# Kernel optimization log

Hardware: AMD Instinct MI355X
Metric: run time of the kernel (lower is better)

Reference implementation:

```python
import jax, jax.numpy as jnp
import numpy as np

def setup_inputs() -> dict:
    key = jax.random.key(0)
    k0, k1, k2, k3 = jax.random.split(key, 4)
    B, L, D, E, Dg = 2, 2048, 2048, 8, 256  # Dg = D // E
    x = jax.random.normal(k0, (B, L, D), dtype=jnp.float32)
    Wg = jax.random.normal(k1, (E, D), dtype=jnp.float32) * 0.02     # gate: Linear(D, E)
    Wd = jax.random.normal(k2, (E, Dg, D), dtype=jnp.float32) * 0.02  # down: Linear(D, Dg) per expert
    Wu = jax.random.normal(k3, (E, D, Dg), dtype=jnp.float32) * 0.02  # up:   Linear(Dg, D) per expert
    return {"x": x, "Wg": Wg, "Wd": Wd, "Wu": Wu, "k": 2}

def reference(x, Wg, Wd, Wu, k):
    B, L, D = x.shape
    E = Wg.shape[0]
    T = B * L
    xf = x.reshape(T, D)
    # gate scores: sigmoid(x @ Wg^T), then top-k gate values G and expert indices I
    S = jax.nn.sigmoid(xf @ Wg.T)            # [T, E]
    G, I = jax.lax.top_k(S, k)               # [T, k], [T, k]
    # combine weights per token per expert (zero for unselected experts);
    # equivalent to the original's one_hot + per-expert gather/scatter-add.
    w = jnp.zeros((T, E), x.dtype).at[jnp.arange(T)[:, None], I].add(G)  # [T, E]
    # down: sum_e w[t,e] * (Wd[e] @ x[t])
    down = jnp.einsum('te,egd,td->tg', w, Wd, xf)   # [T, Dg]
    # inner model is identity
    # up: sum_e w[t,e] * (Wu[e] @ down[t])
    up = jnp.einsum('te,edg,tg->td', w, Wu, down)   # [T, D]
    return up.reshape(B, L, D)
```

## Files before the change

### kernel.cpp

```cpp
#include <hip/hip_runtime.h>
#include <hip/hip_bf16.h>
#include <stdint.h>

#define T_TOK 4096
#define DIM   2048
#define NEXP  8
#define DG    256
#define TOPK  2

#define BM 64
#define BN 128
#define BK 32
#define NROWS  (T_TOK*TOPK + NEXP*BM)
#define NBLK_M (NROWS/BM)

typedef __attribute__((ext_vector_type(8))) short short8;
typedef __attribute__((ext_vector_type(4))) float f32x4;

static __device__ __forceinline__ short f2bf(float f) {
    union { float f; uint32_t u; } v{f};
    uint32_t r = v.u + 0x7fffu + ((v.u >> 16) & 1u);
    return (short)(r >> 16);
}
static __device__ __forceinline__ float b2f(short s) {
    union { uint32_t u; float f; } v{((uint32_t)(unsigned short)s) << 16};
    return v.f;
}

#define GLD16(g, l) \
    __builtin_amdgcn_global_load_lds((const __attribute__((address_space(1))) void*)(g), \
                                     (__attribute__((address_space(3))) void*)(l), 16, 0, 0)

__global__ __launch_bounds__(256) void gate_kernel(const float* __restrict__ x,
                                                   const float* __restrict__ Wg,
                                                   int* __restrict__ gidx,
                                                   float* __restrict__ gval,
                                                   short* __restrict__ x_bf)
{
    int token = blockIdx.x * 4 + (threadIdx.x >> 6);
    int lane  = threadIdx.x & 63;
    const float4* xr = (const float4*)(x + (size_t)token * DIM);

    float4 xv[8];
#pragma unroll
    for (int i = 0; i < 8; i++) xv[i] = xr[lane + 64 * i];

    short4* xb = (short4*)(x_bf + (size_t)token * DIM);
#pragma unroll
    for (int i = 0; i < 8; i++) {
        short4 o;
        o.x = f2bf(xv[i].x); o.y = f2bf(xv[i].y);
        o.z = f2bf(xv[i].z); o.w = f2bf(xv[i].w);
        xb[lane + 64 * i] = o;
    }

    float acc[NEXP];
#pragma unroll
    for (int e = 0; e < NEXP; e++) {
        const float4* wr = (const float4*)(Wg + e * DIM);
        float a = 0.0f;
#pragma unroll
        for (int i = 0; i < 8; i++) {
            float4 w = wr[lane + 64 * i];
            a += xv[i].x * w.x + xv[i].y * w.y + xv[i].z * w.z + xv[i].w * w.w;
        }
        acc[e] = a;
    }

#pragma unroll
    for (int m = 1; m < 64; m <<= 1) {
#pragma unroll
        for (int e = 0; e < NEXP; e++) acc[e] += __shfl_xor(acc[e], m, 64);
    }

    if (lane == 0) {
        float sg[NEXP];
#pragma unroll
        for (int e = 0; e < NEXP; e++) sg[e] = 1.0f / (1.0f + expf(-acc[e]));
        int i0 = 0;
#pragma unroll
        for (int e = 1; e < NEXP; e++) if (sg[e] > sg[i0]) i0 = e;
        int i1 = (i0 == 0) ? 1 : 0;
#pragma unroll
        for (int e = 0; e < NEXP; e++) if (e != i0 && e != i1 && sg[e] > sg[i1]) i1 = e;
        gidx[2 * token + 0] = i0;
        gidx[2 * token + 1] = i1;
        gval[2 * token + 0] = sg[i0];
        gval[2 * token + 1] = sg[i1];
    }
}

__global__ __launch_bounds__(256) void convW_kernel(const float* __restrict__ Wd,
                                                    const float* __restrict__ Wu,
                                                    short* __restrict__ Wd_bf,
                                                    short* __restrict__ Wu_bf,
                                                    int n4)
{
    int i = blockIdx.x * 256 + threadIdx.x;
    const float* s; short* d; int j;
    if (i < n4)      { s = Wd; d = Wd_bf; j = i; }
    else             { s = Wu; d = Wu_bf; j = i - n4; if (j >= n4) return; }
    float4 v = ((const float4*)s)[j];
    short4 o;
    o.x = f2bf(v.x); o.y = f2bf(v.y); o.z = f2bf(v.z); o.w = f2bf(v.w);
    ((short4*)d)[j] = o;
}

__global__ __launch_bounds__(1024) void bucket_kernel(const int* __restrict__ gidx,
                                                      int* __restrict__ rowtok,
                                                      int* __restrict__ rowpos,
                                                      int* __restrict__ seg_off)
{
    __shared__ int cnt[NEXP];
    __shared__ int cur[NEXP];
    int tid = threadIdx.x;
    if (tid < NEXP) cnt[tid] = 0;
    __syncthreads();

    for (int t = tid; t < T_TOK; t += 1024) {
        atomicAdd(&cnt[gidx[2 * t + 0]], 1);
        atomicAdd(&cnt[gidx[2 * t + 1]], 1);
    }
    __syncthreads();

    if (tid == 0) {
        int o = 0;
        for (int e = 0; e < NEXP; e++) {
            seg_off[e] = o;
            cur[e] = o;
            o += ((cnt[e] + BM - 1) / BM) * BM;
        }
        seg_off[NEXP] = o;
    }
    __syncthreads();

    for (int r = tid; r < NROWS; r += 1024) rowtok[r] = -1;
    __syncthreads();

    for (int t = tid; t < T_TOK; t += 1024) {
        for (int s = 0; s < TOPK; s++) {
            int e = gidx[2 * t + s];
            int p = atomicAdd(&cur[e], 1);
            rowtok[p] = t;
            rowpos[2 * t + s] = p;
        }
    }
}

template<int K, int Ntot>
__global__ __launch_bounds__(256) void gemm_kernel(const short* __restrict__ A,
                                                   const short* __restrict__ B,
                                                   const int* __restrict__ rowtok,
                                                   const int* __restrict__ seg_off,
                                                   short* __restrict__ C)
{
    __shared__ short As[BM][BK];
    __shared__ short Bs[BN][BK];

    int row0 = blockIdx.x * BM;
    int total = seg_off[NEXP];
    if (row0 >= total) return;
    int e = 0;
    while (row0 >= seg_off[e + 1]) ++e;
    int n0 = blockIdx.y * BN;

    int tid = threadIdx.x;
    int w = tid >> 6, l = tid & 63;

    int ar = (w << 4) + (l >> 2);
    int achunk = (l & 3) ^ ((l >> 3) & 3);
    int ta = rowtok[row0 + ar]; if (ta < 0) ta = 0;
    const short* ag  = A + (size_t)ta * K + achunk * 8;

    const short* be  = B + (size_t)e * Ntot * K + (size_t)n0 * K;
    const short* bg0 = be + (size_t)(((w * 2 + 0) << 4) + (l >> 2)) * K + achunk * 8;
    const short* bg1 = be + (size_t)(((w * 2 + 1) << 4) + (l >> 2)) * K + achunk * 8;

    auto ldsA  = (__attribute__((address_space(3))) void*)&As[w << 4][0];
    auto ldsB0 = (__attribute__((address_space(3))) void*)&Bs[(w * 2 + 0) << 4][0];
    auto ldsB1 = (__attribute__((address_space(3))) void*)&Bs[(w * 2 + 1) << 4][0];

    int mlane = l & 15, qlane = l >> 4;
    int rchunk = ((qlane ^ ((l >> 1) & 3)) << 3);
    int wm = w >> 1, wn = w & 1;
    const short* pA0 = &As[wm * 32 + mlane][rchunk];
    const short* pA1 = pA0 + 16 * BK;
    const short* pB0 = &Bs[wn * 64 + mlane][rchunk];
    const short* pB1 = pB0 + 16 * BK;
    const short* pB2 = pB0 + 32 * BK;
    const short* pB3 = pB0 + 48 * BK;

    f32x4 acc[2][4] = {};

    for (int k0 = 0; k0 < K; k0 += BK) {
        GLD16(ag, ldsA);
        GLD16(bg0, ldsB0);
        GLD16(bg1, ldsB1);
        ag += BK; bg0 += BK; bg1 += BK;
        __syncthreads();

        short8 a0 = *(const short8*)pA0;
        short8 a1 = *(const short8*)pA1;
        short8 b0 = *(const short8*)pB0;
        short8 b1 = *(const short8*)pB1;
        short8 b2 = *(const short8*)pB2;
        short8 b3 = *(const short8*)pB3;

        acc[0][0] = __builtin_amdgcn_mfma_f32_16x16x32_bf16(a0, b0, acc[0][0], 0, 0, 0);
        acc[0][1] = __builtin_amdgcn_mfma_f32_16x16x32_bf16(a0, b1, acc[0][1], 0, 0, 0);
        acc[0][2] = __builtin_amdgcn_mfma_f32_16x16x32_bf16(a0, b2, acc[0][2], 0, 0, 0);
        acc[0][3] = __builtin_amdgcn_mfma_f32_16x16x32_bf16(a0, b3, acc[0][3], 0, 0, 0);
        acc[1][0] = __builtin_amdgcn_mfma_f32_16x16x32_bf16(a1, b0, acc[1][0], 0, 0, 0);
        acc[1][1] = __builtin_amdgcn_mfma_f32_16x16x32_bf16(a1, b1, acc[1][1], 0, 0, 0);
        acc[1][2] = __builtin_amdgcn_mfma_f32_16x16x32_bf16(a1, b2, acc[1][2], 0, 0, 0);
        acc[1][3] = __builtin_amdgcn_mfma_f32_16x16x32_bf16(a1, b3, acc[1][3], 0, 0, 0);
        __syncthreads();
    }

#pragma unroll
    for (int i = 0; i < 2; i++) {
        int rbase = row0 + wm * 32 + i * 16 + qlane * 4;
#pragma unroll
        for (int j = 0; j < 4; j++) {
            int col = n0 + wn * 64 + j * 16 + mlane;
#pragma unroll
            for (int r = 0; r < 4; r++)
                C[(size_t)(rbase + r) * Ntot + col] = f2bf(acc[i][j][r]);
        }
    }
}

__global__ __launch_bounds__(256) void combine1_kernel(const short* __restrict__ dr,
                                                       const int* __restrict__ rowpos,
                                                       const float* __restrict__ gval,
                                                       short* __restrict__ dt)
{
    int t = blockIdx.x, d = threadIdx.x;
    int   p0 = rowpos[2 * t], p1 = rowpos[2 * t + 1];
    float g0 = gval[2 * t],   g1 = gval[2 * t + 1];
    float v = g0 * b2f(dr[(size_t)p0 * DG + d]) + g1 * b2f(dr[(size_t)p1 * DG + d]);
    dt[(size_t)t * DG + d] = f2bf(v);
}

__global__ __launch_bounds__(256) void combine2_kernel(const short* __restrict__ ur,
                                                       const int* __restrict__ rowpos,
                                                       const float* __restrict__ gval,
                                                       float* __restrict__ out)
{
    int i = blockIdx.x * 256 + threadIdx.x;
    int t = i >> 9;
    int c = (i & 511) * 4;
    int   p0 = rowpos[2 * t], p1 = rowpos[2 * t + 1];
    float g0 = gval[2 * t],   g1 = gval[2 * t + 1];
    short4 u0 = *(const short4*)&ur[(size_t)p0 * DIM + c];
    short4 u1 = *(const short4*)&ur[(size_t)p1 * DIM + c];
    float4 o;
    o.x = g0 * b2f(u0.x) + g1 * b2f(u1.x);
    o.y = g0 * b2f(u0.y) + g1 * b2f(u1.y);
    o.z = g0 * b2f(u0.z) + g1 * b2f(u1.z);
    o.w = g0 * b2f(u0.w) + g1 * b2f(u1.w);
    *(float4*)&out[(size_t)t * DIM + c] = o;
}

extern "C" void kernel_launch(void* const* d_in, const int* in_sizes, int n_in,
                              void* d_out, int out_size, void* d_ws, size_t ws_size,
                              hipStream_t stream) {
    const float* x  = (const float*)d_in[0];
    const float* Wg = (const float*)d_in[1];
    const float* Wd = (const float*)d_in[2];
    const float* Wu = (const float*)d_in[3];
    float* out = (float*)d_out;

    char* p = (char*)d_ws;
    int*   gidx    = (int*)(p + 0);
    float* gval    = (float*)(p + 32768);
    int*   rowtok  = (int*)(p + 65536);
    int*   rowpos  = (int*)(p + 100352);
    int*   seg_off = (int*)(p + 133120);
    short* x_bf    = (short*)(p + 133376);
    short* Wd_bf   = (short*)(p + 133376 + 16777216);
    short* Wu_bf   = Wd_bf + 4194304;
    short* dr_bf   = Wu_bf + 4194304;
    short* dt_bf   = dr_bf + (size_t)NROWS * DG;
    short* ur_bf   = dt_bf + (size_t)T_TOK * DG;

    const int W4 = NEXP * DG * DIM / 4;
    gate_kernel<<<T_TOK / 4, 256, 0, stream>>>(x, Wg, gidx, gval, x_bf);
    convW_kernel<<<(2 * W4 + 255) / 256, 256, 0, stream>>>(Wd, Wu, Wd_bf, Wu_bf, W4);
    bucket_kernel<<<1, 1024, 0, stream>>>(gidx, rowtok, rowpos, seg_off);

    gemm_kernel<DIM, DG><<<dim3(NBLK_M, DG / BN), 256, 0, stream>>>(x_bf, Wd_bf, rowtok, seg_off, dr_bf);
    combine1_kernel<<<T_TOK, 256, 0, stream>>>(dr_bf, rowpos, gval, dt_bf);
    gemm_kernel<DG, DIM><<<dim3(NBLK_M, DIM / BN), 256, 0, stream>>>(dt_bf, Wu_bf, rowtok, seg_off, ur_bf);
    combine2_kernel<<<T_TOK * DIM / 4 / 256, 256, 0, stream>>>(ur_bf, rowpos, gval, out);
}
```

Before: 198.9 us.

## Convert weights to bf16 inside GEMM, enlarge M tile, split-K the down GEMM

Removes the separate fp32-to-bf16 weight conversion kernel. Both GEMMs now load fp32 weights through registers and pack them to bf16 while storing to LDS, with a one-step register prefetch. The M tile doubles to 128 rows, so each block computes 4x4 MFMA tiles. The down GEMM is split along K into four fp32 partial planes that the combine1 kernel sums. This saves a full weight-conversion pass and exposes more parallelism in the K=2048 GEMM. The cost is extra fp32 partial traffic, register-path weight loads instead of direct-to-LDS loads, and more padding rows per expert.

```diff
diff --git a/kernel.cpp b/kernel.cpp
--- a/kernel.cpp
+++ b/kernel.cpp
@@ -8,11 +8,12 @@
 #define DG    256
 #define TOPK  2
 
-#define BM 64
+#define BM 128
 #define BN 128
 #define BK 32
 #define NROWS  (T_TOK*TOPK + NEXP*BM)
 #define NBLK_M (NROWS/BM)
+#define KSPLIT 4
 
 typedef __attribute__((ext_vector_type(8))) short short8;
 typedef __attribute__((ext_vector_type(4))) float f32x4;
@@ -25,6 +26,12 @@
 static __device__ __forceinline__ float b2f(short s) {
     union { uint32_t u; float f; } v{((uint32_t)(unsigned short)s) << 16};
     return v.f;
+}
+static __device__ __forceinline__ short8 pack8(float4 a, float4 b) {
+    short8 o;
+    o[0] = f2bf(a.x); o[1] = f2bf(a.y); o[2] = f2bf(a.z); o[3] = f2bf(a.w);
+    o[4] = f2bf(b.x); o[5] = f2bf(b.y); o[6] = f2bf(b.z); o[7] = f2bf(b.w);
+    return o;
 }
 
 #define GLD16(g, l) \
@@ -88,22 +95,6 @@
         gval[2 * token + 0] = sg[i0];
         gval[2 * token + 1] = sg[i1];
     }
-}
-
-__global__ __launch_bounds__(256) void convW_kernel(const float* __restrict__ Wd,
-                                                    const float* __restrict__ Wu,
-                                                    short* __restrict__ Wd_bf,
-                                                    short* __restrict__ Wu_bf,
-                                                    int n4)
-{
-    int i = blockIdx.x * 256 + threadIdx.x;
-    const float* s; short* d; int j;
-    if (i < n4)      { s = Wd; d = Wd_bf; j = i; }
-    else             { s = Wu; d = Wu_bf; j = i - n4; if (j >= n4) return; }
-    float4 v = ((const float4*)s)[j];
-    short4 o;
-    o.x = f2bf(v.x); o.y = f2bf(v.y); o.z = f2bf(v.z); o.w = f2bf(v.w);
-    ((short4*)d)[j] = o;
 }
 
 __global__ __launch_bounds__(1024) void bucket_kernel(const int* __restrict__ gidx,
@@ -147,99 +138,124 @@
     }
 }
 
-template<int K, int Ntot>
+template<int K, int KC, int Ntot, bool PART>
 __global__ __launch_bounds__(256) void gemm_kernel(const short* __restrict__ A,
-                                                   const short* __restrict__ B,
+                                                   const float* __restrict__ Bf,
                                                    const int* __restrict__ rowtok,
                                                    const int* __restrict__ seg_off,
-                                                   short* __restrict__ C)
+                                                   short* __restrict__ Cbf,
+                                                   float* __restrict__ Cf32)
 {
     __shared__ short As[BM][BK];
     __shared__ short Bs[BN][BK];
 
     int row0 = blockIdx.x * BM;
-    int total = seg_off[NEXP];
-    if (row0 >= total) return;
+    if (row0 >= seg_off[NEXP]) return;
     int e = 0;
     while (row0 >= seg_off[e + 1]) ++e;
     int n0 = blockIdx.y * BN;
+    int kb = blockIdx.z;
+    int k_start = kb * KC;
 
     int tid = threadIdx.x;
     int w = tid >> 6, l = tid & 63;
 
-    int ar = (w << 4) + (l >> 2);
-    int achunk = (l & 3) ^ ((l >> 3) & 3);
-    int ta = rowtok[row0 + ar]; if (ta < 0) ta = 0;
-    const short* ag  = A + (size_t)ta * K + achunk * 8;
-
-    const short* be  = B + (size_t)e * Ntot * K + (size_t)n0 * K;
-    const short* bg0 = be + (size_t)(((w * 2 + 0) << 4) + (l >> 2)) * K + achunk * 8;
-    const short* bg1 = be + (size_t)(((w * 2 + 1) << 4) + (l >> 2)) * K + achunk * 8;
-
-    auto ldsA  = (__attribute__((address_space(3))) void*)&As[w << 4][0];
-    auto ldsB0 = (__attribute__((address_space(3))) void*)&Bs[(w * 2 + 0) << 4][0];
-    auto ldsB1 = (__attribute__((address_space(3))) void*)&Bs[(w * 2 + 1) << 4][0];
-
-    int mlane = l & 15, qlane = l >> 4;
-    int rchunk = ((qlane ^ ((l >> 1) & 3)) << 3);
+    int r = l >> 2, c = l & 3;
+    int gch = c ^ ((r >> 1) & 3);
+    int ar0 = w * 16 + r, ar1 = 64 + w * 16 + r;
+    int ta0 = rowtok[row0 + ar0]; if (ta0 < 0) ta0 = 0;
+    int ta1 = rowtok[row0 + ar1]; if (ta1 < 0) ta1 = 0;
+    const short* ag0 = A + (size_t)ta0 * K + k_start + gch * 8;
+    const short* ag1 = A + (size_t)ta1 * K + k_start + gch * 8;
+    auto ldsA0 = (__attribute__((address_space(3))) void*)&As[w * 16][0];
+    auto ldsA1 = (__attribute__((address_space(3))) void*)&As[64 + w * 16][0];
+
+    int bn = tid >> 1, h = tid & 1;
+    const float4* bg = (const float4*)(Bf + (size_t)e * Ntot * K
+                                          + (size_t)(n0 + bn) * K + k_start + h * 16);
+    int sw = (bn >> 1) & 3;
+    short* bs0 = &Bs[bn][((2 * h + 0) ^ sw) * 8];
+    short* bs1 = &Bs[bn][((2 * h + 1) ^ sw) * 8];
+
+    int mlane = l & 15, q = l >> 4;
+    int rA = (q ^ ((mlane >> 1) & 3)) * 8;
     int wm = w >> 1, wn = w & 1;
-    const short* pA0 = &As[wm * 32 + mlane][rchunk];
-    const short* pA1 = pA0 + 16 * BK;
-    const short* pB0 = &Bs[wn * 64 + mlane][rchunk];
-    const short* pB1 = pB0 + 16 * BK;
-    const short* pB2 = pB0 + 32 * BK;
-    const short* pB3 = pB0 + 48 * BK;
-
-    f32x4 acc[2][4] = {};
-
-    for (int k0 = 0; k0 < K; k0 += BK) {
-        GLD16(ag, ldsA);
-        GLD16(bg0, ldsB0);
-        GLD16(bg1, ldsB1);
-        ag += BK; bg0 += BK; bg1 += BK;
+    const short* pA = &As[wm * 64 + mlane][0] + rA;
+    const short* pB = &Bs[wn * 64 + mlane][0] + rA;
+
+    f32x4 acc[4][4] = {};
+
+    float4 br0 = bg[0], br1 = bg[1], br2 = bg[2], br3 = bg[3];
+    bg += 8;
+
+    constexpr int NS = KC / BK;
+    for (int t = 0; t < NS; ++t) {
+        GLD16(ag0, ldsA0);
+        GLD16(ag1, ldsA1);
+        ag0 += BK; ag1 += BK;
+
+        *(short8*)bs0 = pack8(br0, br1);
+        *(short8*)bs1 = pack8(br2, br3);
+        if (t + 1 < NS) { br0 = bg[0]; br1 = bg[1]; br2 = bg[2]; br3 = bg[3]; bg += 8; }
         __syncthreads();
 
-        short8 a0 = *(const short8*)pA0;
-        short8 a1 = *(const short8*)pA1;
-        short8 b0 = *(const short8*)pB0;
-        short8 b1 = *(const short8*)pB1;
-        short8 b2 = *(const short8*)pB2;
-        short8 b3 = *(const short8*)pB3;
-
-        acc[0][0] = __builtin_amdgcn_mfma_f32_16x16x32_bf16(a0, b0, acc[0][0], 0, 0, 0);
-        acc[0][1] = __builtin_amdgcn_mfma_f32_16x16x32_bf16(a0, b1, acc[0][1], 0, 0, 0);
-        acc[0][2] = __builtin_amdgcn_mfma_f32_16x16x32_bf16(a0, b2, acc[0][2], 0, 0, 0);
-        acc[0][3] = __builtin_amdgcn_mfma_f32_16x16x32_bf16(a0, b3, acc[0][3], 0, 0, 0);
-        acc[1][0] = __builtin_amdgcn_mfma_f32_16x16x32_bf16(a1, b0, acc[1][0], 0, 0, 0);
-        acc[1][1] = __builtin_amdgcn_mfma_f32_16x16x32_bf16(a1, b1, acc[1][1], 0, 0, 0);
-        acc[1][2] = __builtin_amdgcn_mfma_f32_16x16x32_bf16(a1, b2, acc[1][2], 0, 0, 0);
-        acc[1][3] = __builtin_amdgcn_mfma_f32_16x16x32_bf16(a1, b3, acc[1][3], 0, 0, 0);
+        short8 a[4], b[4];
+#pragma unroll
+        for (int i = 0; i < 4; i++) a[i] = *(const short8*)(pA + i * 16 * BK);
+#pragma unroll
+        for (int j = 0; j < 4; j++) b[j] = *(const short8*)(pB + j * 16 * BK);
+
+#pragma unroll
+        for (int i = 0; i < 4; i++)
+#pragma unroll
+            for (int j = 0; j < 4; j++)
+                acc[i][j] = __builtin_amdgcn_mfma_f32_16x16x32_bf16(a[i], b[j], acc[i][j], 0, 0, 0);
         __syncthreads();
     }
 
 #pragma unroll
-    for (int i = 0; i < 2; i++) {
-        int rbase = row0 + wm * 32 + i * 16 + qlane * 4;
+    for (int i = 0; i < 4; i++) {
+        int rbase = row0 + wm * 64 + i * 16 + q * 4;
 #pragma unroll
         for (int j = 0; j < 4; j++) {
             int col = n0 + wn * 64 + j * 16 + mlane;
 #pragma unroll
-            for (int r = 0; r < 4; r++)
-                C[(size_t)(rbase + r) * Ntot + col] = f2bf(acc[i][j][r]);
+            for (int rr = 0; rr < 4; rr++) {
+                if (PART)
+                    Cf32[((size_t)kb * NROWS + (rbase + rr)) * Ntot + col] = acc[i][j][rr];
+                else
+                    Cbf[(size_t)(rbase + rr) * Ntot + col] = f2bf(acc[i][j][rr]);
+            }
         }
     }
 }
 
-__global__ __launch_bounds__(256) void combine1_kernel(const short* __restrict__ dr,
+__global__ __launch_bounds__(256) void combine1_kernel(const float* __restrict__ P,
                                                        const int* __restrict__ rowpos,
                                                        const float* __restrict__ gval,
                                                        short* __restrict__ dt)
 {
-    int t = blockIdx.x, d = threadIdx.x;
+    int t = blockIdx.x * 4 + (threadIdx.x >> 6);
+    int d = threadIdx.x & 63;
     int   p0 = rowpos[2 * t], p1 = rowpos[2 * t + 1];
     float g0 = gval[2 * t],   g1 = gval[2 * t + 1];
-    float v = g0 * b2f(dr[(size_t)p0 * DG + d]) + g1 * b2f(dr[(size_t)p1 * DG + d]);
-    dt[(size_t)t * DG + d] = f2bf(v);
+    const float4* P4 = (const float4*)P;
+    const size_t plane = (size_t)NROWS * DG / 4;
+
+    float4 s0 = {0, 0, 0, 0}, s1 = {0, 0, 0, 0};
+#pragma unroll
+    for (int kb = 0; kb < KSPLIT; kb++) {
+        float4 a = P4[kb * plane + (size_t)p0 * (DG / 4) + d];
+        float4 b = P4[kb * plane + (size_t)p1 * (DG / 4) + d];
+        s0.x += a.x; s0.y += a.y; s0.z += a.z; s0.w += a.w;
+        s1.x += b.x; s1.y += b.y; s1.z += b.z; s1.w += b.w;
+    }
+    short4 o;
+    o.x = f2bf(g0 * s0.x + g1 * s1.x);
+    o.y = f2bf(g0 * s0.y + g1 * s1.y);
+    o.z = f2bf(g0 * s0.z + g1 * s1.z);
+    o.w = f2bf(g0 * s0.w + g1 * s1.w);
+    ((short4*)(dt + (size_t)t * DG))[d] = o;
 }
 
 __global__ __launch_bounds__(256) void combine2_kernel(const short* __restrict__ ur,
@@ -275,22 +291,23 @@
     int*   gidx    = (int*)(p + 0);
     float* gval    = (float*)(p + 32768);
     int*   rowtok  = (int*)(p + 65536);
-    int*   rowpos  = (int*)(p + 100352);
-    int*   seg_off = (int*)(p + 133120);
-    short* x_bf    = (short*)(p + 133376);
-    short* Wd_bf   = (short*)(p + 133376 + 16777216);
-    short* Wu_bf   = Wd_bf + 4194304;
-    short* dr_bf   = Wu_bf + 4194304;
-    short* dt_bf   = dr_bf + (size_t)NROWS * DG;
-    short* ur_bf   = dt_bf + (size_t)T_TOK * DG;
-
-    const int W4 = NEXP * DG * DIM / 4;
+    int*   rowpos  = (int*)(p + 102400);
+    int*   seg_off = (int*)(p + 135168);
+    short* x_bf    = (short*)(p + 135424);
+    float* dr_part = (float*)(p + 16912640);
+    short* dt_bf   = (short*)(p + 54661376);
+    short* ur_bf   = (short*)(p + 56758528);
+
     gate_kernel<<<T_TOK / 4, 256, 0, stream>>>(x, Wg, gidx, gval, x_bf);
-    convW_kernel<<<(2 * W4 + 255) / 256, 256, 0, stream>>>(Wd, Wu, Wd_bf, Wu_bf, W4);
     bucket_kernel<<<1, 1024, 0, stream>>>(gidx, rowtok, rowpos, seg_off);
 
-    gemm_kernel<DIM, DG><<<dim3(NBLK_M, DG / BN), 256, 0, stream>>>(x_bf, Wd_bf, rowtok, seg_off, dr_bf);
-    combine1_kernel<<<T_TOK, 256, 0, stream>>>(dr_bf, rowpos, gval, dt_bf);
-    gemm_kernel<DG, DIM><<<dim3(NBLK_M, DIM / BN), 256, 0, stream>>>(dt_bf, Wu_bf, rowtok, seg_off, ur_bf);
+    gemm_kernel<DIM, DIM / KSPLIT, DG, true>
+        <<<dim3(NBLK_M, DG / BN, KSPLIT), 256, 0, stream>>>(
+            x_bf, Wd, rowtok, seg_off, nullptr, dr_part);
+    combine1_kernel<<<T_TOK / 4, 256, 0, stream>>>(dr_part, rowpos, gval, dt_bf);
+
+    gemm_kernel<DG, DG, DIM, false>
+        <<<dim3(NBLK_M, DIM / BN, 1), 256, 0, stream>>>(
+            dt_bf, Wu, rowtok, seg_off, ur_bf, nullptr);
     combine2_kernel<<<T_TOK * DIM / 4 / 256, 256, 0, stream>>>(ur_bf, rowpos, gval, out);
 }
```

After: 210.0 us. 5.6% more time.
